# Performance work log

Measured on AMD Instinct MI355X. Metric: run time of the kernel, lower is better.

The kernel has to match this reference:

```python
import jax, jax.numpy as jnp
import numpy as np

N = 20000      # nodes
E = 320000     # edges (no self loops; PyG adds them with fill_value='mean')
FIN = 16       # node feature dim
ED = 22        # edge feature dim
NEG_SLOPE = 0.2


def _lin(k, i, o):
    return (jax.random.normal(k, (i, o)) * (1.0 / np.sqrt(i))).astype(jnp.float32)


def setup_inputs() -> dict:
    key = jax.random.key(0)
    ks = jax.random.split(key, 32)
    x = jax.random.normal(ks[0], (N, FIN), dtype=jnp.float32)
    src = jax.random.randint(ks[1], (E,), 0, N, dtype=jnp.int32)
    off = jax.random.randint(ks[2], (E,), 1, N, dtype=jnp.int32)
    dst = (src + off) % N  # guarantees no pre-existing self loops
    edge_index = jnp.stack([src, dst], axis=0)
    edge_attr = jax.random.normal(ks[3], (E, ED), dtype=jnp.float32)

    def conv_params(kbase, fin, H, C):
        k = jax.random.split(kbase, 6)
        return dict(
            W=_lin(k[0], fin, H * C),
            att_s=jax.random.normal(k[1], (H, C), dtype=jnp.float32) * 0.1,
            att_d=jax.random.normal(k[2], (H, C), dtype=jnp.float32) * 0.1,
            We=_lin(k[3], ED, H * C),
            att_e=jax.random.normal(k[4], (H, C), dtype=jnp.float32) * 0.1,
            b=jnp.zeros((H * C,), dtype=jnp.float32),
        )

    p1 = conv_params(ks[4], FIN, 8, 32)
    p2 = conv_params(ks[5], 256, 8, 32)
    p3 = conv_params(ks[6], 256, 12, 64)
    Wf = _lin(ks[7], 256 + 256 + 768, 1)
    bf = jnp.zeros((1,), dtype=jnp.float32)
    return {
        'x': x, 'edge_index': edge_index, 'edge_attr': edge_attr,
        'W1': p1['W'], 'as1': p1['att_s'], 'ad1': p1['att_d'], 'We1': p1['We'], 'ae1': p1['att_e'], 'b1': p1['b'],
        'W2': p2['W'], 'as2': p2['att_s'], 'ad2': p2['att_d'], 'We2': p2['We'], 'ae2': p2['att_e'], 'b2': p2['b'],
        'W3': p3['W'], 'as3': p3['att_s'], 'ad3': p3['att_d'], 'We3': p3['We'], 'ae3': p3['att_e'], 'b3': p3['b'],
        'Wf': Wf, 'bf': bf,
    }


def _add_self_loops_mean(src, dst, edge_attr):
    # PyG add_self_loops(fill_value='mean'): self-loop edge_attr = mean of
    # incoming edge_attr at each node (0 for isolated nodes).
    cnt = jax.ops.segment_sum(jnp.ones((E,), jnp.float32), dst, N)  # [N]
    mean_ea = jax.ops.segment_sum(edge_attr, dst, N) / jnp.maximum(cnt, 1.0)[:, None]
    loop = jnp.arange(N, dtype=src.dtype)
    src_f = jnp.concatenate([src, loop])
    dst_f = jnp.concatenate([dst, loop])
    ea_f = jnp.concatenate([edge_attr, mean_ea], axis=0)
    return src_f, dst_f, ea_f


def _gat_conv(x, src, dst, ea, W, att_s, att_d, We, att_e, b, H, C):
    # node/edge projections
    h = (x @ W).reshape(-1, H, C)                  # [N,H,C]
    e = (ea @ We).reshape(-1, H, C)                # [E',H,C]
    a_s = jnp.sum(h * att_s, axis=-1)              # [N,H]
    a_d = jnp.sum(h * att_d, axis=-1)              # [N,H]
    a_e = jnp.sum(e * att_e, axis=-1)              # [E',H]
    alpha = a_s[src] + a_d[dst] + a_e              # [E',H]
    alpha = jax.nn.leaky_relu(alpha, NEG_SLOPE)
    # segment softmax over edges sharing a destination node
    amax = jax.ops.segment_max(alpha, dst, N)      # every node has a self loop
    ex = jnp.exp(alpha - amax[dst])
    denom = jax.ops.segment_sum(ex, dst, N)
    w = ex / denom[dst]                            # [E',H]
    out = jax.ops.segment_sum(w[:, :, None] * h[src], dst, N)  # [N,H,C]
    return out.reshape(-1, H * C) + b


def reference(x, edge_index, edge_attr,
              W1, as1, ad1, We1, ae1, b1,
              W2, as2, ad2, We2, ae2, b2,
              W3, as3, ad3, We3, ae3, b3,
              Wf, bf):
    src, dst = edge_index[0], edge_index[1]
    src_f, dst_f, ea_f = _add_self_loops_mean(src, dst, edge_attr)
    x1 = jax.nn.relu(_gat_conv(x, src_f, dst_f, ea_f, W1, as1, ad1, We1, ae1, b1, 8, 32))
    x2 = jax.nn.relu(_gat_conv(x1, src_f, dst_f, ea_f, W2, as2, ad2, We2, ae2, b2, 8, 32))
    x3 = jax.nn.relu(_gat_conv(x2, src_f, dst_f, ea_f, W3, as3, ad3, We3, ae3, b3, 12, 64))
    xc = jnp.concatenate([x1, x2, x3], axis=1)     # [N,1280]
    return jax.nn.sigmoid(xc @ Wf + bf)
```

## Files before the change

### kernel.cpp

```cpp
#include <hip/hip_runtime.h>

#define NN 20000
#define EE 320000
#define EF 340000
#define EDIM 22
#define NBLK ((NN + 255) / 256)

typedef short bf16x8 __attribute__((ext_vector_type(8)));
typedef float f32x4 __attribute__((ext_vector_type(4)));

__device__ __forceinline__ float blo(unsigned u) {
  union { unsigned x; float f; } v; v.x = u << 16; return v.f;
}
__device__ __forceinline__ float bhi(unsigned u) {
  union { unsigned x; float f; } v; v.x = u & 0xffff0000u; return v.f;
}
__device__ __forceinline__ ushort f2b(float f) {
  union { float f; unsigned u; } v;
  v.f = f;
  unsigned u = v.u;
  return (ushort)((u + 0x7fffu + ((u >> 16) & 1u)) >> 16);
}
__device__ __forceinline__ float lrelu(float a) { return a > 0.f ? a : 0.2f * a; }


__global__ void count_deg_kernel(const int* __restrict__ dst, int* __restrict__ cnt) {
  int e = blockIdx.x * blockDim.x + threadIdx.x;
  if (e < EE) atomicAdd(&cnt[dst[e]], 1);
}

__global__ void scan1_kernel(const int* __restrict__ cnt, int* __restrict__ off,
                             int* __restrict__ btot) {
  __shared__ int wsum[4];
  const int b = blockIdx.x, tid = threadIdx.x;
  const int lane = tid & 63, w = tid >> 6;
  const int i = b * 256 + tid;
  int v = (i < NN) ? (cnt[i] + 1) : 0;
  int x = v;
#pragma unroll
  for (int s = 1; s < 64; s <<= 1) {
    int t = __shfl_up(x, s);
    if (lane >= s) x += t;
  }
  if (lane == 63) wsum[w] = x;
  __syncthreads();
  if (tid == 0) {
    int a = 0;
#pragma unroll
    for (int k = 0; k < 4; ++k) { int t = wsum[k]; wsum[k] = a; a += t; }
  }
  __syncthreads();
  int excl = wsum[w] + x - v;
  if (i < NN) off[i] = excl;
  if (tid == 255) btot[b] = wsum[3] + x;
}

__global__ void scan2_kernel(int* __restrict__ btot) {
  __shared__ int s0;
  const int tid = threadIdx.x, lane = tid & 63, w = tid >> 6;
  int v = (tid < NBLK) ? btot[tid] : 0;
  int x = v;
#pragma unroll
  for (int s = 1; s < 64; s <<= 1) {
    int t = __shfl_up(x, s);
    if (lane >= s) x += t;
  }
  if (w == 0 && lane == 63) s0 = x;
  __syncthreads();
  int excl = x - v + (w ? s0 : 0);
  if (tid < NBLK) btot[tid] = excl;
}

__global__ void scan3_kernel(int* __restrict__ off, const int* __restrict__ btot,
                             int* __restrict__ cursor) {
  const int i = blockIdx.x * blockDim.x + threadIdx.x;
  if (i < NN) {
    int o = off[i] + btot[i >> 8];
    off[i] = o;
    cursor[i] = o;
  }
  if (i == 0) off[NN] = EF;
}

__global__ void scatter_kernel(const int* __restrict__ src, const int* __restrict__ dst,
                               int* __restrict__ cursor, int* __restrict__ csr_src,
                               int* __restrict__ csr_dst, int* __restrict__ csr_eid) {
  int e = blockIdx.x * blockDim.x + threadIdx.x;
  if (e >= EF) return;
  int s, d;
  if (e < EE) { s = src[e]; d = dst[e]; } else { s = e - EE; d = s; }
  int pos = atomicAdd(&cursor[d], 1);
  csr_src[pos] = s;
  csr_dst[pos] = d;
  csr_eid[pos] = e;
}

__global__ __launch_bounds__(256) void mean_ea_kernel(
    const int* __restrict__ off, const int* __restrict__ csr_eid,
    const float* __restrict__ edge_attr, float* __restrict__ mean_ea) {
  const int n = (int)((blockIdx.x * blockDim.x + threadIdx.x) >> 6);
  const int lane = threadIdx.x & 63;
  if (n >= NN) return;
  const int start = off[n], end = off[n + 1];
  float a[24];
#pragma unroll
  for (int d = 0; d < 24; ++d) a[d] = 0.f;
  for (int j = start + lane; j < end; j += 64) {
    int eid = csr_eid[j];
    if (eid < EE) {
      const float* ea = edge_attr + (size_t)eid * EDIM;
      float4 q0 = *(const float4*)(ea + 0);
      float4 q1 = *(const float4*)(ea + 4);
      float4 q2 = *(const float4*)(ea + 8);
      float4 q3 = *(const float4*)(ea + 12);
      float4 q4 = *(const float4*)(ea + 16);
      float2 q5 = *(const float2*)(ea + 20);
      a[0] += q0.x; a[1] += q0.y; a[2] += q0.z; a[3] += q0.w;
      a[4] += q1.x; a[5] += q1.y; a[6] += q1.z; a[7] += q1.w;
      a[8] += q2.x; a[9] += q2.y; a[10] += q2.z; a[11] += q2.w;
      a[12] += q3.x; a[13] += q3.y; a[14] += q3.z; a[15] += q3.w;
      a[16] += q4.x; a[17] += q4.y; a[18] += q4.z; a[19] += q4.w;
      a[20] += q5.x; a[21] += q5.y;
    }
  }
#pragma unroll
  for (int s = 32; s > 0; s >>= 1)
#pragma unroll
    for (int d = 0; d < EDIM; ++d) a[d] += __shfl_xor(a[d], s);
  if (lane == 0) {
    const float den = 1.f / fmaxf((float)(end - start - 1), 1.f);
    float* mp = mean_ea + (size_t)n * EDIM;
#pragma unroll
    for (int d = 0; d < EDIM; ++d) mp[d] = a[d] * den;
  }
}

__global__ void ea_csr_kernel(const int* __restrict__ csr_eid,
                              const float* __restrict__ edge_attr,
                              const float* __restrict__ mean_ea,
                              ushort* __restrict__ ea_csr) {
  int t = blockIdx.x * blockDim.x + threadIdx.x;
  if (t >= EF * 11) return;
  int j = t / 11, dp = t % 11;
  int eid = csr_eid[j];
  const float* ea = (eid < EE) ? edge_attr + (size_t)eid * EDIM
                               : mean_ea + (size_t)(eid - EE) * EDIM;
  float2 v = *(const float2*)(ea + dp * 2);
  unsigned u = (unsigned)f2b(v.x) | ((unsigned)f2b(v.y) << 16);
  *(unsigned*)(ea_csr + (size_t)j * EDIM + dp * 2) = u;
}


__global__ void cvt_x_kernel(const float* __restrict__ x, ushort* __restrict__ ab) {
  int t = blockIdx.x * blockDim.x + threadIdx.x;
  if (t >= NN * 32) return;
  int n = t >> 5, c = t & 31;
  ab[t] = (c < 16) ? f2b(x[n * 16 + c]) : (ushort)0;
}

__global__ void prep_weights_kernel(
    const float* __restrict__ W1, const float* __restrict__ W2, const float* __restrict__ W3,
    ushort* __restrict__ wt1, ushort* __restrict__ wt2, ushort* __restrict__ wt3,
    const float* __restrict__ We1, const float* __restrict__ ate1, float* __restrict__ wec1,
    const float* __restrict__ We2, const float* __restrict__ ate2, float* __restrict__ wec2,
    const float* __restrict__ We3, const float* __restrict__ ate3, float* __restrict__ wec3) {
  int t = blockIdx.x * blockDim.x + threadIdx.x;
  const int S0 = 256 * 32, S1 = 256 * 256, S2 = 768 * 256;
  const int S3 = EDIM * 8, S4 = EDIM * 8, S5 = EDIM * 12;
  if (t < S0) {
    int nc = t >> 5, k = t & 31;
    wt1[t] = (k < 16) ? f2b(W1[(size_t)k * 256 + nc]) : (ushort)0;
    return;
  }
  t -= S0;
  if (t < S1) {
    int nc = t >> 8, k = t & 255;
    wt2[t] = f2b(W2[(size_t)k * 256 + nc]);
    return;
  }
  t -= S1;
  if (t < S2) {
    int nc = t >> 8, k = t & 255;
    wt3[t] = f2b(W3[(size_t)k * 768 + nc]);
    return;
  }
  t -= S2;
  if (t < S3) {
    int d = t / 8, h = t % 8;
    float v = 0.f;
    for (int c = 0; c < 32; ++c) v += We1[(size_t)d * 256 + h * 32 + c] * ate1[h * 32 + c];
    wec1[t] = v;
    return;
  }
  t -= S3;
  if (t < S4) {
    int d = t / 8, h = t % 8;
    float v = 0.f;
    for (int c = 0; c < 32; ++c) v += We2[(size_t)d * 256 + h * 32 + c] * ate2[h * 32 + c];
    wec2[t] = v;
    return;
  }
  t -= S4;
  if (t < S5) {
    int d = t / 12, h = t % 12;
    float v = 0.f;
    for (int c = 0; c < 64; ++c) v += We3[(size_t)d * 768 + h * 64 + c] * ate3[h * 64 + c];
    wec3[t] = v;
  }
}

template <int K, int CDIM>
__global__ __launch_bounds__(256) void gemm_lds_kernel(
    const ushort* __restrict__ A, const ushort* __restrict__ Bt,
    ushort* __restrict__ C, const float* __restrict__ atts,
    const float* __restrict__ attd, float* __restrict__ a_s,
    float* __restrict__ a_d, int M, int Nc, int H) {
  constexpr int CPC = K / 8;
  constexpr int SWZ = (CPC - 1) < 7 ? (CPC - 1) : 7;
  __shared__ __align__(16) ushort Blds[64 * K];
  const int tid = threadIdx.x;
  const int lane = tid & 63;
  const int wid = tid >> 6;
  const int bn = blockIdx.x * 64;
  const int bm = blockIdx.y * 128 + wid * 32;
  const int r = lane & 15;
  const int kg = lane >> 4;

#pragma unroll
  for (int it = 0; it < (64 * CPC) / 256; ++it) {
    int idx = it * 256 + tid;
    int col = idx / CPC;
    int c = idx % CPC;
    const uint4 v = *(const uint4*)(Bt + (size_t)(bn + col) * K + c * 8);
    *(uint4*)(&Blds[(col * CPC + (c ^ (col & SWZ))) * 8]) = v;
  }
  __syncthreads();

  const int row0 = bm + r, row1 = bm + 16 + r;
  const bool v0 = row0 < M, v1 = row1 < M;
  const ushort* ap0 = A + (size_t)row0 * K + kg * 8;
  const ushort* ap1 = A + (size_t)row1 * K + kg * 8;

  f32x4 acc[2][4] = {};
#pragma unroll
  for (int k0 = 0; k0 < K; k0 += 32) {
    bf16x8 a0 = {}, a1 = {};
    if (v0) a0 = *(const bf16x8*)(ap0 + k0);
    if (v1) a1 = *(const bf16x8*)(ap1 + k0);
    const int cbase = k0 / 8 + kg;
#pragma unroll
    for (int nf = 0; nf < 4; ++nf) {
      const int col = nf * 16 + r;
      bf16x8 bfr = *(const bf16x8*)(&Blds[(col * CPC + (cbase ^ (col & SWZ))) * 8]);
      acc[0][nf] = __builtin_amdgcn_mfma_f32_16x16x32_bf16(a0, bfr, acc[0][nf], 0, 0, 0);
      acc[1][nf] = __builtin_amdgcn_mfma_f32_16x16x32_bf16(a1, bfr, acc[1][nf], 0, 0, 0);
    }
  }
#pragma unroll
  for (int half = 0; half < 2; ++half)
#pragma unroll
    for (int nf = 0; nf < 4; ++nf)
#pragma unroll
      for (int reg = 0; reg < 4; ++reg) {
        int row = bm + half * 16 + kg * 4 + reg;
        if (row < M) C[(size_t)row * Nc + bn + nf * 16 + r] = f2b(acc[half][nf][reg]);
      }

  float as_v[4], ad_v[4];
#pragma unroll
  for (int nf = 0; nf < 4; ++nf) {
    int cg = bn + nf * 16 + r;
    as_v[nf] = atts[cg];
    ad_v[nf] = attd[cg];
  }
  const int h0g = bn / CDIM;
#pragma unroll
  for (int half = 0; half < 2; ++half) {
#pragma unroll
    for (int reg = 0; reg < 4; ++reg) {
      float sA, dA, sB = 0.f, dB = 0.f;
      if (CDIM == 32) {
        sA = acc[half][0][reg] * as_v[0] + acc[half][1][reg] * as_v[1];
        dA = acc[half][0][reg] * ad_v[0] + acc[half][1][reg] * ad_v[1];
        sB = acc[half][2][reg] * as_v[2] + acc[half][3][reg] * as_v[3];
        dB = acc[half][2][reg] * ad_v[2] + acc[half][3][reg] * ad_v[3];
      } else {
        sA = acc[half][0][reg] * as_v[0] + acc[half][1][reg] * as_v[1] +
             acc[half][2][reg] * as_v[2] + acc[half][3][reg] * as_v[3];
        dA = acc[half][0][reg] * ad_v[0] + acc[half][1][reg] * ad_v[1] +
             acc[half][2][reg] * ad_v[2] + acc[half][3][reg] * ad_v[3];
      }
#pragma unroll
      for (int s = 8; s >= 1; s >>= 1) {
        sA += __shfl_xor(sA, s);
        dA += __shfl_xor(dA, s);
        if (CDIM == 32) { sB += __shfl_xor(sB, s); dB += __shfl_xor(dB, s); }
      }
      if (r == 0) {
        int row = bm + half * 16 + kg * 4 + reg;
        if (row < M) {
          a_s[row * H + h0g] = sA;
          a_d[row * H + h0g] = dA;
          if (CDIM == 32) {
            a_s[row * H + h0g + 1] = sB;
            a_d[row * H + h0g + 1] = dB;
          }
        }
      }
    }
  }
}

__global__ void ase_kernel(const int* __restrict__ csr_src, const int* __restrict__ csr_dst,
                           const ushort* __restrict__ ea_csr, const float* __restrict__ wec,
                           const float* __restrict__ a_s, const float* __restrict__ a_d,
                           float* __restrict__ wexp, int H) {
  int t = blockIdx.x * blockDim.x + threadIdx.x;
  if (t >= EF * H) return;
  int j = t / H, hh = t % H;
  const ushort* ea = ea_csr + (size_t)j * EDIM;
  float v = 0.f;
#pragma unroll
  for (int d = 0; d < 11; ++d) {
    unsigned u = *(const unsigned*)(ea + 2 * d);
    v += blo(u) * wec[(2 * d) * H + hh] + bhi(u) * wec[(2 * d + 1) * H + hh];
  }
  v += a_s[csr_src[j] * H + hh] + a_d[csr_dst[j] * H + hh];
  wexp[t] = __expf(lrelu(v));
}

template <int H, int C, int NCH, bool WRITE_X>
__global__ __launch_bounds__(256) void aggregate_kernel(
    const float* __restrict__ wexp, const ushort* __restrict__ hb,
    const int* __restrict__ off, const int* __restrict__ csr_src,
    const float* __restrict__ bias, ushort* __restrict__ xb,
    const float* __restrict__ WfL, float* __restrict__ logitpart, int slotbase) {
  constexpr int HC = H * C;
  constexpr int CHUNK = HC / NCH;
  constexpr int FPL = CHUNK / 64;
  const int t = (int)((blockIdx.x * blockDim.x + threadIdx.x) >> 6);
  const int lane = threadIdx.x & 63;
  const int n = t / NCH, ch = t - n * NCH;
  if (n >= NN) return;
  const int start = off[n], end = off[n + 1];
  const int f0 = ch * CHUNK + lane * FPL;
  const int qh = f0 / C;
  const ushort* hrow = hb + f0;
  const float* wp = wexp + qh;

  float acc[FPL] = {};
  float dn = 0.f;
  int j = start;
  for (; j + 4 <= end; j += 4) {
    int s0 = csr_src[j], s1 = csr_src[j + 1], s2 = csr_src[j + 2], s3 = csr_src[j + 3];
    float w0 = wp[(size_t)j * H];
    float w1 = wp[(size_t)(j + 1) * H];
    float w2 = wp[(size_t)(j + 2) * H];
    float w3 = wp[(size_t)(j + 3) * H];
    uint2 u0 = *(const uint2*)(hrow + (size_t)s0 * HC);
    uint2 u1 = *(const uint2*)(hrow + (size_t)s1 * HC);
    uint2 u2 = *(const uint2*)(hrow + (size_t)s2 * HC);
    uint2 u3 = *(const uint2*)(hrow + (size_t)s3 * HC);
    dn += (w0 + w1) + (w2 + w3);
    acc[0] += w0 * blo(u0.x) + w1 * blo(u1.x) + w2 * blo(u2.x) + w3 * blo(u3.x);
    acc[1] += w0 * bhi(u0.x) + w1 * bhi(u1.x) + w2 * bhi(u2.x) + w3 * bhi(u3.x);
    acc[2] += w0 * blo(u0.y) + w1 * blo(u1.y) + w2 * blo(u2.y) + w3 * blo(u3.y);
    acc[3] += w0 * bhi(u0.y) + w1 * bhi(u1.y) + w2 * bhi(u2.y) + w3 * bhi(u3.y);
  }
  for (; j < end; ++j) {
    int s0 = csr_src[j];
    float w0 = wp[(size_t)j * H];
    uint2 u0 = *(const uint2*)(hrow + (size_t)s0 * HC);
    dn += w0;
    acc[0] += w0 * blo(u0.x);
    acc[1] += w0 * bhi(u0.x);
    acc[2] += w0 * blo(u0.y);
    acc[3] += w0 * bhi(u0.y);
  }

  const float my_rd = 1.f / dn;
  const float4 wf4 = *(const float4*)(WfL + f0);
  const float wfv[4] = {wf4.x, wf4.y, wf4.z, wf4.w};
  float o[FPL];
  float partial = 0.f;
#pragma unroll
  for (int i = 0; i < FPL; ++i) {
    o[i] = fmaxf(acc[i] * my_rd + bias[f0 + i], 0.f);
    partial += o[i] * wfv[i];
  }
  if (WRITE_X) {
    uint2 pk;
    pk.x = (unsigned)f2b(o[0]) | ((unsigned)f2b(o[1]) << 16);
    pk.y = (unsigned)f2b(o[2]) | ((unsigned)f2b(o[3]) << 16);
    *(uint2*)(xb + (size_t)n * HC + f0) = pk;
  }
#pragma unroll
  for (int s = 32; s > 0; s >>= 1) partial += __shfl_xor(partial, s);
  if (lane == 0) logitpart[n * 5 + slotbase + ch] = partial;
}

__global__ void final_sigmoid_kernel(const float* __restrict__ logitpart,
                                     const float* __restrict__ bf,
                                     float* __restrict__ out) {
  int n = blockIdx.x * blockDim.x + threadIdx.x;
  if (n >= NN) return;
  const float* lp = logitpart + n * 5;
  float s = lp[0] + lp[1] + lp[2] + lp[3] + lp[4] + bf[0];
  out[n] = 1.f / (1.f + __expf(-s));
}


extern "C" void kernel_launch(void* const* d_in, const int* in_sizes, int n_in,
                              void* d_out, int out_size, void* d_ws, size_t ws_size,
                              hipStream_t stream) {
  const float* x     = (const float*)d_in[0];
  const int*   eidx  = (const int*)d_in[1];
  const float* eattr = (const float*)d_in[2];
  const float* W[3]   = {(const float*)d_in[3],  (const float*)d_in[9],  (const float*)d_in[15]};
  const float* ats[3] = {(const float*)d_in[4],  (const float*)d_in[10], (const float*)d_in[16]};
  const float* atd[3] = {(const float*)d_in[5],  (const float*)d_in[11], (const float*)d_in[17]};
  const float* We[3]  = {(const float*)d_in[6],  (const float*)d_in[12], (const float*)d_in[18]};
  const float* ate[3] = {(const float*)d_in[7],  (const float*)d_in[13], (const float*)d_in[19]};
  const float* bb[3]  = {(const float*)d_in[8],  (const float*)d_in[14], (const float*)d_in[20]};
  const float* Wf = (const float*)d_in[21];
  const float* bf = (const float*)d_in[22];
  float* out = (float*)d_out;

  const int* src = eidx;
  const int* dst = eidx + EE;

  char* p = (char*)d_ws;
  auto carve = [&](size_t bytes) -> char* {
    char* q = p;
    p += (bytes + 255) & ~(size_t)255;
    return q;
  };
  ushort* x1b    = (ushort*)carve((size_t)NN * 256 * 2);
  ushort* x2b    = (ushort*)carve((size_t)NN * 256 * 2);
  ushort* hbuf   = (ushort*)carve((size_t)NN * 768 * 2);
  ushort* abf1   = (ushort*)carve((size_t)NN * 32 * 2);
  ushort* wt1    = (ushort*)carve((size_t)256 * 32 * 2);
  ushort* wt2    = (ushort*)carve((size_t)256 * 256 * 2);
  ushort* wt3    = (ushort*)carve((size_t)768 * 256 * 2);
  ushort* ea_csr = (ushort*)carve((size_t)EF * EDIM * 2);
  float*  a_s    = (float*)carve((size_t)NN * 12 * 4);
  float*  a_d    = (float*)carve((size_t)NN * 12 * 4);
  float*  wexp   = (float*)carve((size_t)EF * 12 * 4);
  float*  mea    = (float*)carve((size_t)NN * EDIM * 4);
  float*  wec1   = (float*)carve((size_t)EDIM * 8 * 4);
  float*  wec2   = (float*)carve((size_t)EDIM * 8 * 4);
  float*  wec3   = (float*)carve((size_t)EDIM * 12 * 4);
  float*  lpart  = (float*)carve((size_t)NN * 5 * 4);
  int* cnt       = (int*)carve((size_t)NN * 4);
  int* off       = (int*)carve((size_t)(NN + 1) * 4);
  int* btot      = (int*)carve((size_t)NBLK * 4);
  int* cursor    = (int*)carve((size_t)NN * 4);
  int* csr_src   = (int*)carve((size_t)EF * 4);
  int* csr_dst   = (int*)carve((size_t)EF * 4);
  int* csr_eid   = (int*)carve((size_t)EF * 4);

  hipMemsetAsync(cnt, 0, (size_t)NN * 4, stream);
  count_deg_kernel<<<(EE + 255) / 256, 256, 0, stream>>>(dst, cnt);
  scan1_kernel<<<NBLK, 256, 0, stream>>>(cnt, off, btot);
  scan2_kernel<<<1, 128, 0, stream>>>(btot);
  scan3_kernel<<<NBLK, 256, 0, stream>>>(off, btot, cursor);
  scatter_kernel<<<(EF + 255) / 256, 256, 0, stream>>>(src, dst, cursor, csr_src, csr_dst,
                                                       csr_eid);
  mean_ea_kernel<<<(NN * 64 + 255) / 256, 256, 0, stream>>>(off, csr_eid, eattr, mea);
  ea_csr_kernel<<<(EF * 11 + 255) / 256, 256, 0, stream>>>(csr_eid, eattr, mea, ea_csr);

  cvt_x_kernel<<<(NN * 32 + 255) / 256, 256, 0, stream>>>(x, abf1);
  {
    const int total = 256 * 32 + 256 * 256 + 768 * 256 + EDIM * 8 + EDIM * 8 + EDIM * 12;
    prep_weights_kernel<<<(total + 255) / 256, 256, 0, stream>>>(
        W[0], W[1], W[2], wt1, wt2, wt3,
        We[0], ate[0], wec1, We[1], ate[1], wec2, We[2], ate[2], wec3);
  }

  const int Hs[3] = {8, 8, 12};
  const ushort* Ain[3] = {abf1, x1b, x2b};
  const ushort* Wt[3] = {wt1, wt2, wt3};
  float* wecL[3] = {wec1, wec2, wec3};
  ushort* xoutb[3] = {x1b, x2b, nullptr};
  const float* WfL[3] = {Wf, Wf + 256, Wf + 512};
  const int slotb[3] = {0, 1, 2};

  for (int L = 0; L < 3; ++L) {
    const int H = Hs[L];
    const int HC = (L < 2) ? 256 : 768;
    dim3 g(HC / 64, (NN + 127) / 128);
    if (L == 0)
      gemm_lds_kernel<32, 32><<<g, 256, 0, stream>>>(Ain[L], Wt[L], hbuf, ats[L], atd[L],
                                                     a_s, a_d, NN, HC, H);
    else if (L == 1)
      gemm_lds_kernel<256, 32><<<g, 256, 0, stream>>>(Ain[L], Wt[L], hbuf, ats[L], atd[L],
                                                      a_s, a_d, NN, HC, H);
    else
      gemm_lds_kernel<256, 64><<<g, 256, 0, stream>>>(Ain[L], Wt[L], hbuf, ats[L], atd[L],
                                                      a_s, a_d, NN, HC, H);
    ase_kernel<<<(EF * H + 255) / 256, 256, 0, stream>>>(csr_src, csr_dst, ea_csr, wecL[L],
                                                         a_s, a_d, wexp, H);
    if (H == 8) {
      int blocks = (NN * 1 + 3) / 4;
      aggregate_kernel<8, 32, 1, true><<<blocks, 256, 0, stream>>>(
          wexp, hbuf, off, csr_src, bb[L], xoutb[L], WfL[L], lpart, slotb[L]);
    } else {
      int blocks = (NN * 3 + 3) / 4;
      aggregate_kernel<12, 64, 3, false><<<blocks, 256, 0, stream>>>(
          wexp, hbuf, off, csr_src, bb[L], xoutb[L], WfL[L], lpart, slotb[L]);
    }
  }

  final_sigmoid_kernel<<<(NN + 255) / 256, 256, 0, stream>>>(lpart, bf, out);
}
```

Measured before the change: 342.1 us.

## Fuse mean edge-attr and bf16 CSR build; per-edge ase with all heads

Merges the mean-edge-attr reduction and the bf16 CSR edge-attr conversion into one per-node kernel that writes each edge row while accumulating the mean, then writes the self-loop row. This drops the fp32 mean buffer and one full pass over edge_attr. The x conversion is folded into the weight-prep launch to remove a kernel launch. The attention-score kernel now uses one thread per edge for all heads with vectorized loads and stores, templated on H, instead of one thread per edge-head pair that reread the edge attributes H times. In exchange, per-thread register use rises and parallelism drops, and the fused CSR writes follow CSR order per node.

```diff
diff --git a/kernel.cpp b/kernel.cpp
--- a/kernel.cpp
+++ b/kernel.cpp
@@ -95,9 +95,9 @@
   csr_eid[pos] = e;
 }
 
-__global__ __launch_bounds__(256) void mean_ea_kernel(
+__global__ __launch_bounds__(256) void ea_build_kernel(
     const int* __restrict__ off, const int* __restrict__ csr_eid,
-    const float* __restrict__ edge_attr, float* __restrict__ mean_ea) {
+    const float* __restrict__ edge_attr, ushort* __restrict__ ea_csr) {
   const int n = (int)((blockIdx.x * blockDim.x + threadIdx.x) >> 6);
   const int lane = threadIdx.x & 63;
   if (n >= NN) return;
@@ -105,68 +105,68 @@
   float a[24];
 #pragma unroll
   for (int d = 0; d < 24; ++d) a[d] = 0.f;
+  int selfj = -1;
   for (int j = start + lane; j < end; j += 64) {
     int eid = csr_eid[j];
     if (eid < EE) {
       const float* ea = edge_attr + (size_t)eid * EDIM;
+      float r[22];
       float4 q0 = *(const float4*)(ea + 0);
       float4 q1 = *(const float4*)(ea + 4);
       float4 q2 = *(const float4*)(ea + 8);
       float4 q3 = *(const float4*)(ea + 12);
       float4 q4 = *(const float4*)(ea + 16);
       float2 q5 = *(const float2*)(ea + 20);
-      a[0] += q0.x; a[1] += q0.y; a[2] += q0.z; a[3] += q0.w;
-      a[4] += q1.x; a[5] += q1.y; a[6] += q1.z; a[7] += q1.w;
-      a[8] += q2.x; a[9] += q2.y; a[10] += q2.z; a[11] += q2.w;
-      a[12] += q3.x; a[13] += q3.y; a[14] += q3.z; a[15] += q3.w;
-      a[16] += q4.x; a[17] += q4.y; a[18] += q4.z; a[19] += q4.w;
-      a[20] += q5.x; a[21] += q5.y;
+      r[0] = q0.x; r[1] = q0.y; r[2] = q0.z; r[3] = q0.w;
+      r[4] = q1.x; r[5] = q1.y; r[6] = q1.z; r[7] = q1.w;
+      r[8] = q2.x; r[9] = q2.y; r[10] = q2.z; r[11] = q2.w;
+      r[12] = q3.x; r[13] = q3.y; r[14] = q3.z; r[15] = q3.w;
+      r[16] = q4.x; r[17] = q4.y; r[18] = q4.z; r[19] = q4.w;
+      r[20] = q5.x; r[21] = q5.y;
+#pragma unroll
+      for (int d = 0; d < EDIM; ++d) a[d] += r[d];
+      ushort* op = ea_csr + (size_t)j * EDIM;
+#pragma unroll
+      for (int d = 0; d < 11; ++d) {
+        unsigned u = (unsigned)f2b(r[2 * d]) | ((unsigned)f2b(r[2 * d + 1]) << 16);
+        *(unsigned*)(op + 2 * d) = u;
+      }
+    } else {
+      selfj = j;
     }
   }
 #pragma unroll
   for (int s = 32; s > 0; s >>= 1)
 #pragma unroll
     for (int d = 0; d < EDIM; ++d) a[d] += __shfl_xor(a[d], s);
-  if (lane == 0) {
+  if (selfj >= 0) {
     const float den = 1.f / fmaxf((float)(end - start - 1), 1.f);
-    float* mp = mean_ea + (size_t)n * EDIM;
-#pragma unroll
-    for (int d = 0; d < EDIM; ++d) mp[d] = a[d] * den;
-  }
-}
-
-__global__ void ea_csr_kernel(const int* __restrict__ csr_eid,
-                              const float* __restrict__ edge_attr,
-                              const float* __restrict__ mean_ea,
-                              ushort* __restrict__ ea_csr) {
-  int t = blockIdx.x * blockDim.x + threadIdx.x;
-  if (t >= EF * 11) return;
-  int j = t / 11, dp = t % 11;
-  int eid = csr_eid[j];
-  const float* ea = (eid < EE) ? edge_attr + (size_t)eid * EDIM
-                               : mean_ea + (size_t)(eid - EE) * EDIM;
-  float2 v = *(const float2*)(ea + dp * 2);
-  unsigned u = (unsigned)f2b(v.x) | ((unsigned)f2b(v.y) << 16);
-  *(unsigned*)(ea_csr + (size_t)j * EDIM + dp * 2) = u;
-}
-
-
-__global__ void cvt_x_kernel(const float* __restrict__ x, ushort* __restrict__ ab) {
-  int t = blockIdx.x * blockDim.x + threadIdx.x;
-  if (t >= NN * 32) return;
-  int n = t >> 5, c = t & 31;
-  ab[t] = (c < 16) ? f2b(x[n * 16 + c]) : (ushort)0;
+    ushort* op = ea_csr + (size_t)selfj * EDIM;
+#pragma unroll
+    for (int d = 0; d < 11; ++d) {
+      unsigned u = (unsigned)f2b(a[2 * d] * den) | ((unsigned)f2b(a[2 * d + 1] * den) << 16);
+      *(unsigned*)(op + 2 * d) = u;
+    }
+  }
 }
 
 __global__ void prep_weights_kernel(
+    const float* __restrict__ x, ushort* __restrict__ ab,
     const float* __restrict__ W1, const float* __restrict__ W2, const float* __restrict__ W3,
     ushort* __restrict__ wt1, ushort* __restrict__ wt2, ushort* __restrict__ wt3,
     const float* __restrict__ We1, const float* __restrict__ ate1, float* __restrict__ wec1,
     const float* __restrict__ We2, const float* __restrict__ ate2, float* __restrict__ wec2,
     const float* __restrict__ We3, const float* __restrict__ ate3, float* __restrict__ wec3) {
   int t = blockIdx.x * blockDim.x + threadIdx.x;
+  const int SX = NN * 32;
   const int S0 = 256 * 32, S1 = 256 * 256, S2 = 768 * 256;
   const int S3 = EDIM * 8, S4 = EDIM * 8, S5 = EDIM * 12;
+  if (t < SX) {
+    int n = t >> 5, c = t & 31;
+    ab[t] = (c < 16) ? f2b(x[n * 16 + c]) : (ushort)0;
+    return;
+  }
+  t -= SX;
   if (t < S0) {
     int nc = t >> 5, k = t & 31;
     wt1[t] = (k < 16) ? f2b(W1[(size_t)k * 256 + nc]) : (ushort)0;
@@ -311,22 +311,49 @@
   }
 }
 
+template <int H>
 __global__ void ase_kernel(const int* __restrict__ csr_src, const int* __restrict__ csr_dst,
                            const ushort* __restrict__ ea_csr, const float* __restrict__ wec,
                            const float* __restrict__ a_s, const float* __restrict__ a_d,
-                           float* __restrict__ wexp, int H) {
-  int t = blockIdx.x * blockDim.x + threadIdx.x;
-  if (t >= EF * H) return;
-  int j = t / H, hh = t % H;
-  const ushort* ea = ea_csr + (size_t)j * EDIM;
-  float v = 0.f;
+                           float* __restrict__ wexp) {
+  int j = blockIdx.x * blockDim.x + threadIdx.x;
+  if (j >= EF) return;
+  const ushort* eap = ea_csr + (size_t)j * EDIM;
+  float ea[22];
 #pragma unroll
   for (int d = 0; d < 11; ++d) {
-    unsigned u = *(const unsigned*)(ea + 2 * d);
-    v += blo(u) * wec[(2 * d) * H + hh] + bhi(u) * wec[(2 * d + 1) * H + hh];
-  }
-  v += a_s[csr_src[j] * H + hh] + a_d[csr_dst[j] * H + hh];
-  wexp[t] = __expf(lrelu(v));
+    unsigned u = *(const unsigned*)(eap + 2 * d);
+    ea[2 * d] = blo(u);
+    ea[2 * d + 1] = bhi(u);
+  }
+  const float* asp = a_s + (size_t)csr_src[j] * H;
+  const float* adp = a_d + (size_t)csr_dst[j] * H;
+  float v[H];
+#pragma unroll
+  for (int q = 0; q < H / 4; ++q) {
+    float4 s4 = *(const float4*)(asp + q * 4);
+    float4 d4 = *(const float4*)(adp + q * 4);
+    v[q * 4 + 0] = s4.x + d4.x;
+    v[q * 4 + 1] = s4.y + d4.y;
+    v[q * 4 + 2] = s4.z + d4.z;
+    v[q * 4 + 3] = s4.w + d4.w;
+  }
+#pragma unroll
+  for (int d = 0; d < EDIM; ++d) {
+    const float* wr = wec + d * H;
+#pragma unroll
+    for (int h = 0; h < H; ++h) v[h] += ea[d] * wr[h];
+  }
+  float* op = wexp + (size_t)j * H;
+#pragma unroll
+  for (int q = 0; q < H / 4; ++q) {
+    float4 o;
+    o.x = __expf(lrelu(v[q * 4 + 0]));
+    o.y = __expf(lrelu(v[q * 4 + 1]));
+    o.z = __expf(lrelu(v[q * 4 + 2]));
+    o.w = __expf(lrelu(v[q * 4 + 3]));
+    *(float4*)(op + q * 4) = o;
+  }
 }
 
 template <int H, int C, int NCH, bool WRITE_X>
@@ -446,7 +473,6 @@
   float*  a_s    = (float*)carve((size_t)NN * 12 * 4);
   float*  a_d    = (float*)carve((size_t)NN * 12 * 4);
   float*  wexp   = (float*)carve((size_t)EF * 12 * 4);
-  float*  mea    = (float*)carve((size_t)NN * EDIM * 4);
   float*  wec1   = (float*)carve((size_t)EDIM * 8 * 4);
   float*  wec2   = (float*)carve((size_t)EDIM * 8 * 4);
   float*  wec3   = (float*)carve((size_t)EDIM * 12 * 4);
@@ -466,18 +492,16 @@
   scan3_kernel<<<NBLK, 256, 0, stream>>>(off, btot, cursor);
   scatter_kernel<<<(EF + 255) / 256, 256, 0, stream>>>(src, dst, cursor, csr_src, csr_dst,
                                                        csr_eid);
-  mean_ea_kernel<<<(NN * 64 + 255) / 256, 256, 0, stream>>>(off, csr_eid, eattr, mea);
-  ea_csr_kernel<<<(EF * 11 + 255) / 256, 256, 0, stream>>>(csr_eid, eattr, mea, ea_csr);
-
-  cvt_x_kernel<<<(NN * 32 + 255) / 256, 256, 0, stream>>>(x, abf1);
+  ea_build_kernel<<<(NN * 64 + 255) / 256, 256, 0, stream>>>(off, csr_eid, eattr, ea_csr);
+
   {
-    const int total = 256 * 32 + 256 * 256 + 768 * 256 + EDIM * 8 + EDIM * 8 + EDIM * 12;
+    const int total = NN * 32 + 256 * 32 + 256 * 256 + 768 * 256 +
+                      EDIM * 8 + EDIM * 8 + EDIM * 12;
     prep_weights_kernel<<<(total + 255) / 256, 256, 0, stream>>>(
-        W[0], W[1], W[2], wt1, wt2, wt3,
+        x, abf1, W[0], W[1], W[2], wt1, wt2, wt3,
         We[0], ate[0], wec1, We[1], ate[1], wec2, We[2], ate[2], wec3);
   }
 
-  const int Hs[3] = {8, 8, 12};
   const ushort* Ain[3] = {abf1, x1b, x2b};
   const ushort* Wt[3] = {wt1, wt2, wt3};
   float* wecL[3] = {wec1, wec2, wec3};
@@ -486,7 +510,7 @@
   const int slotb[3] = {0, 1, 2};
 
   for (int L = 0; L < 3; ++L) {
-    const int H = Hs[L];
+    const int H = (L < 2) ? 8 : 12;
     const int HC = (L < 2) ? 256 : 768;
     dim3 g(HC / 64, (NN + 127) / 128);
     if (L == 0)
@@ -498,8 +522,12 @@
     else
       gemm_lds_kernel<256, 64><<<g, 256, 0, stream>>>(Ain[L], Wt[L], hbuf, ats[L], atd[L],
                                                       a_s, a_d, NN, HC, H);
-    ase_kernel<<<(EF * H + 255) / 256, 256, 0, stream>>>(csr_src, csr_dst, ea_csr, wecL[L],
-                                                         a_s, a_d, wexp, H);
+    if (H == 8)
+      ase_kernel<8><<<(EF + 255) / 256, 256, 0, stream>>>(csr_src, csr_dst, ea_csr,
+                                                          wecL[L], a_s, a_d, wexp);
+    else
+      ase_kernel<12><<<(EF + 255) / 256, 256, 0, stream>>>(csr_src, csr_dst, ea_csr,
+                                                           wecL[L], a_s, a_d, wexp);
     if (H == 8) {
       int blocks = (NN * 1 + 3) / 4;
       aggregate_kernel<8, 32, 1, true><<<blocks, 256, 0, stream>>>(
```

Result: faster. 308.4 us (-9.9%).
